# Kernel optimization log

Measured on AMD Instinct MI355X. Metric: run time of the kernel, lower is better.

## Reference

```python
import jax, jax.numpy as jnp
import numpy as np
from jax import lax

LBDA = 0.1
EPS = 0.01
NUM_CLASSES = 20


def setup_inputs() -> dict:
    key = jax.random.key(0)
    k1, k2 = jax.random.split(key)
    target_features = jax.random.normal(k1, (2048, 8, 2048), dtype=jnp.float32)
    support_features = jax.random.normal(k2, (100, 8, 2048), dtype=jnp.float32)
    # 20-way 5-shot: every class present so per-class mean is well defined
    support_labels = jnp.repeat(jnp.arange(NUM_CLASSES, dtype=jnp.int32), 100 // NUM_CLASSES)
    return {
        "target_features": target_features,
        "support_features": support_features,
        "support_labels": support_labels,
    }


def _softmin(xs, lbda):
    # -lbda * log(sum_i exp(-x_i/lbda)), stable
    return -lbda * jax.nn.logsumexp(jnp.stack([-x / lbda for x in xs], axis=0), axis=0)


def otam_cum_dist(dists, lbda=LBDA):
    # dists: [Q, Sp, L, S] frame distance matrices
    d = jnp.pad(dists, ((0, 0), (0, 0), (0, 0), (1, 1)))  # pad columns -> M = S + 2
    M = d.shape[-1]
    # row 0: running sum along columns (cum[0,0] = d[0,0] = 0 from padding)
    row0 = jnp.cumsum(d[:, :, 0, :], axis=-1)

    def step(prev_row, d_row):
        # prev_row, d_row: [Q, Sp, M]; column 0 is never written -> stays 0
        cur = [jnp.zeros_like(d_row[..., 0])]
        cur.append(d_row[..., 1] + _softmin([prev_row[..., 0], prev_row[..., 1], cur[0]], lbda))
        for m in range(2, M - 1):
            cur.append(d_row[..., m] + _softmin([prev_row[..., m - 1], cur[m - 1]], lbda))
        cur.append(d_row[..., M - 1] + _softmin([prev_row[..., M - 2], prev_row[..., M - 1], cur[M - 2]], lbda))
        new_row = jnp.stack(cur, axis=-1)
        return new_row, None

    d_rows = jnp.moveaxis(d[:, :, 1:, :], 2, 0)  # [L-1, Q, Sp, M]
    final_row, _ = lax.scan(step, row0, d_rows)
    return final_row[..., -1]  # [Q, Sp]


def cos_sim(x, y, eps=EPS):
    num = x @ y.T
    den = jnp.linalg.norm(x, axis=-1)[:, None] * jnp.linalg.norm(y, axis=-1)[None, :] + eps
    return num / den


def reference(target_features, support_features, support_labels):
    Q, S, D = target_features.shape
    Sp = support_features.shape[0]
    tf = target_features.reshape(Q * S, D)
    sf = support_features.reshape(Sp * S, D)
    frame_dists = 1.0 - cos_sim(tf, sf)  # [Q*S, Sp*S]
    # '(tb ts) (sb ss) -> tb sb ts ss'
    dists = frame_dists.reshape(Q, S, Sp, S).transpose(0, 2, 1, 3)
    cum_dists = otam_cum_dist(dists) + otam_cum_dist(dists.transpose(0, 1, 3, 2))  # [Q, Sp]
    # per-class mean over support (torch.unique returns sorted labels 0..C-1)
    onehot = (support_labels[:, None] == jnp.arange(NUM_CLASSES)[None, :]).astype(cum_dists.dtype)
    onehot = onehot / jnp.sum(onehot, axis=0, keepdims=True)
    class_dists = cum_dists @ onehot  # [Q, C]
    return -class_dists[None]  # logits [1, Q, C]
```

## Files before the change

kernel.cpp:

```cpp
#include <hip/hip_runtime.h>

#define QN    2048
#define SS    8
#define DD    2048
#define SP    100
#define NCLS  20
#define MROWS (QN*SS)
#define NREAL (SP*SS)
#define NPAD  1024
#define KK    DD
#define BK    64
#define NTK   (KK/BK)

typedef __bf16 bf16x8 __attribute__((ext_vector_type(8)));
typedef float  f32x4  __attribute__((ext_vector_type(4)));

__device__ __forceinline__ unsigned short f2bf(float f) {
    unsigned int u = __float_as_uint(f);
    u += 0x7fffu + ((u >> 16) & 1u);
    return (unsigned short)(u >> 16);
}

__global__ void cvt_kernel(const float* __restrict__ tf, const float* __restrict__ sf,
                           unsigned short* __restrict__ Abf, unsigned short* __restrict__ Bbf,
                           float* __restrict__ nA, float* __restrict__ nB,
                           float* __restrict__ out)
{
    if (blockIdx.x < 160) out[blockIdx.x * 256 + threadIdx.x] = 0.f;

    const int wv   = threadIdx.x >> 6;
    const int lane = threadIdx.x & 63;
    const int row  = blockIdx.x * 4 + wv;

    const float* src;
    unsigned short* dst;
    float* nrm; int r;
    if (row < MROWS) { src = tf + (size_t)row * DD; dst = Abf + (size_t)row * DD; nrm = nA; r = row; }
    else {
        r = row - MROWS;
        if (r >= NREAL) {
            unsigned short* d2 = Bbf + (size_t)r * DD;
            ushort4 z = make_ushort4(0, 0, 0, 0);
#pragma unroll
            for (int j = 0; j < 8; ++j) *(ushort4*)(d2 + j * 256 + lane * 4) = z;
            if (lane == 0) nB[r] = 0.f;
            return;
        }
        src = sf + (size_t)r * DD; dst = Bbf + (size_t)r * DD; nrm = nB;
    }

    float s = 0.f;
#pragma unroll
    for (int j = 0; j < 8; j++) {
        float4 v = *(const float4*)(src + j * 256 + lane * 4);
        s += v.x*v.x + v.y*v.y + v.z*v.z + v.w*v.w;
        ushort4 pk = make_ushort4(f2bf(v.x), f2bf(v.y), f2bf(v.z), f2bf(v.w));
        *(ushort4*)(dst + j * 256 + lane * 4) = pk;
    }
#pragma unroll
    for (int o = 32; o; o >>= 1) s += __shfl_down(s, o);
    if (lane == 0) nrm[r] = sqrtf(s);
}

__device__ __forceinline__ float softmin2(float a, float b) {
    float mn = fminf(a, b), mx = fmaxf(a, b);
    return mn - 0.1f * __logf(1.0f + __expf((mn - mx) * 10.0f));
}
__device__ __forceinline__ float softmin3(float a, float b, float c) {
    float mn = fminf(fminf(a, b), c);
    float sum = __expf((mn - a) * 10.0f) + __expf((mn - b) * 10.0f) + __expf((mn - c) * 10.0f);
    return mn - 0.1f * __logf(sum);
}

__device__ __forceinline__ void gld16(const void* g, void* l) {
    __builtin_amdgcn_global_load_lds(
        (const __attribute__((address_space(1))) unsigned int*)g,
        (__attribute__((address_space(3))) unsigned int*)l, 16, 0, 0);
}

__device__ __forceinline__ float cellf(const uint4* raw, int a, int b) {
    const unsigned* p = (const unsigned*)raw;
    unsigned wv = p[a * 4 + (b >> 1)];
    return __uint_as_float((b & 1) ? (wv & 0xffff0000u) : (wv << 16));
}

__device__ __forceinline__ float otam_dp(const uint4* raw, int dir) {
    float prev[10], cur[10];
    prev[0] = 0.f;
#pragma unroll
    for (int m = 1; m <= 8; m++) {
        float v0 = cellf(raw, 0, m - 1), v1 = cellf(raw, m - 1, 0);
        prev[m] = prev[m - 1] + (dir ? v1 : v0);
    }
    prev[9] = prev[8];
#pragma unroll
    for (int l = 1; l < 8; l++) {
        float d[8];
#pragma unroll
        for (int j = 0; j < 8; j++) {
            float v0 = cellf(raw, l, j), v1 = cellf(raw, j, l);
            d[j] = dir ? v1 : v0;
        }
        cur[1] = d[0] + softmin3(prev[0], prev[1], 0.0f);
#pragma unroll
        for (int m = 2; m <= 8; m++)
            cur[m] = d[m - 1] + softmin2(prev[m - 1], cur[m - 1]);
        cur[9] = softmin3(prev[8], prev[9], cur[8]);
#pragma unroll
        for (int m = 1; m < 10; m++) prev[m] = cur[m];
    }
    return prev[9];
}

template<int CB>
__device__ __forceinline__ void tile_body(
    char* lds8, f32x4 (&acc)[8][4],
    const unsigned short* sA, const unsigned short* sB,
    const int t, const int arow, const int brow, const int sb16, const int stoff)
{
    constexpr int NB = CB ^ 65536;
    const bool st = (t + 1 < NTK);
    const int t1 = (t + 1) * BK;
    bf16x8 bf0[4], bf1[4];

    if (st) {
        gld16(sB + t1,                    lds8 + NB + 32768 + stoff);
        gld16(sB + (size_t) 64 * KK + t1, lds8 + NB + 32768 +  8192 + stoff);
        gld16(sB + (size_t)128 * KK + t1, lds8 + NB + 32768 + 16384 + stoff);
        gld16(sB + (size_t)192 * KK + t1, lds8 + NB + 32768 + 24576 + stoff);
        gld16(sA + t1,                    lds8 + NB + stoff);
        gld16(sA + (size_t)128 * KK + t1, lds8 + NB + 16384 + stoff);
    }

    {
        bf16x8 af0[4], af1[4];
#pragma unroll
        for (int i = 0; i < 4; ++i)
            af0[i] = *(const bf16x8*)(lds8 + CB + arow + i * 2048 + sb16);
#pragma unroll
        for (int n = 0; n < 4; ++n)
            bf0[n] = *(const bf16x8*)(lds8 + CB + brow + n * 2048 + sb16);
#pragma unroll
        for (int i = 0; i < 4; ++i)
            af1[i] = *(const bf16x8*)(lds8 + CB + arow + i * 2048 + (sb16 ^ 64));
#pragma unroll
        for (int n = 0; n < 4; ++n)
            bf1[n] = *(const bf16x8*)(lds8 + CB + brow + n * 2048 + (sb16 ^ 64));
        __builtin_amdgcn_s_setprio(1);
#pragma unroll
        for (int mi = 0; mi < 4; ++mi)
#pragma unroll
            for (int n = 0; n < 4; ++n)
                acc[mi][n] = __builtin_amdgcn_mfma_f32_16x16x32_bf16(af0[mi], bf0[n], acc[mi][n], 0, 0, 0);
#pragma unroll
        for (int mi = 0; mi < 4; ++mi)
#pragma unroll
            for (int n = 0; n < 4; ++n)
                acc[mi][n] = __builtin_amdgcn_mfma_f32_16x16x32_bf16(af1[mi], bf1[n], acc[mi][n], 0, 0, 0);
        __builtin_amdgcn_s_setprio(0);
    }

    if (st) asm volatile("s_waitcnt vmcnt(6)");
    else    asm volatile("s_waitcnt vmcnt(0)");
    __builtin_amdgcn_s_barrier();

    if (st) {
        gld16(sA + (size_t) 64 * KK + t1, lds8 + NB +  8192 + stoff);
        gld16(sA + (size_t)192 * KK + t1, lds8 + NB + 24576 + stoff);
    }

    {
        bf16x8 af2[4], af3[4];
#pragma unroll
        for (int i = 0; i < 4; ++i)
            af2[i] = *(const bf16x8*)(lds8 + CB + arow + 8192 + i * 2048 + sb16);
#pragma unroll
        for (int i = 0; i < 4; ++i)
            af3[i] = *(const bf16x8*)(lds8 + CB + arow + 8192 + i * 2048 + (sb16 ^ 64));
        __builtin_amdgcn_s_setprio(1);
#pragma unroll
        for (int mi = 0; mi < 4; ++mi)
#pragma unroll
            for (int n = 0; n < 4; ++n)
                acc[4 + mi][n] = __builtin_amdgcn_mfma_f32_16x16x32_bf16(af2[mi], bf0[n], acc[4 + mi][n], 0, 0, 0);
#pragma unroll
        for (int mi = 0; mi < 4; ++mi)
#pragma unroll
            for (int n = 0; n < 4; ++n)
                acc[4 + mi][n] = __builtin_amdgcn_mfma_f32_16x16x32_bf16(af3[mi], bf1[n], acc[4 + mi][n], 0, 0, 0);
        __builtin_amdgcn_s_setprio(0);
    }

    if (st) asm volatile("s_waitcnt vmcnt(2)");
    __builtin_amdgcn_s_barrier();
}

__global__ __launch_bounds__(512, 2) void gemm_kernel(
    const unsigned short* __restrict__ A,
    const unsigned short* __restrict__ B,
    const float* __restrict__ nA, const float* __restrict__ nB,
    const int* __restrict__ labels,
    float* __restrict__ out)
{
    extern __shared__ __align__(16) char lds8[];

    const int mt   = blockIdx.x;
    const int nt   = blockIdx.y;
    const int tid  = threadIdx.x;
    const int lane = tid & 63;
    const int w    = tid >> 6;
    const int wm   = w >> 2, wn = w & 3;
    const int col  = lane & 15, kg = lane >> 4;
    const int mbase = mt * 256, nbase = nt * 256;

    const int ks8 = ((lane & 7) ^ (lane >> 3)) << 3;
    const unsigned short* sA = A + (size_t)(mbase + w * 8 + (lane >> 3)) * KK + ks8;
    const unsigned short* sB = B + (size_t)(nbase + w * 8 + (lane >> 3)) * KK + ks8;
    const int stoff = w * 1024 + lane * 16;

    const int sb16 = ((kg ^ (col & 7)) << 4);
    const int arow = (wm * 128 + col) * 128;
    const int brow = 32768 + (wn * 64 + col) * 128;

    f32x4 acc[8][4] = {};

    gld16(sB,                       lds8 + 32768 + stoff);
    gld16(sB + (size_t) 64 * KK,    lds8 + 32768 +  8192 + stoff);
    gld16(sB + (size_t)128 * KK,    lds8 + 32768 + 16384 + stoff);
    gld16(sB + (size_t)192 * KK,    lds8 + 32768 + 24576 + stoff);
    gld16(sA,                       lds8 + stoff);
    gld16(sA + (size_t)128 * KK,    lds8 + 16384 + stoff);
    gld16(sA + (size_t) 64 * KK,    lds8 +  8192 + stoff);
    gld16(sA + (size_t)192 * KK,    lds8 + 24576 + stoff);
    asm volatile("s_waitcnt vmcnt(0)");
    __builtin_amdgcn_s_barrier();

    for (int t = 0; t < NTK; t += 2) {
        tile_body<0>    (lds8, acc, sA, sB, t,     arow, brow, sb16, stoff);
        tile_body<65536>(lds8, acc, sA, sB, t + 1, arow, brow, sb16, stoff);
    }

    __syncthreads();
    unsigned short* eb = (unsigned short*)lds8 + w * 2304;
    const int pr  = lane & 31;
    const int qv2 = pr >> 3, sv = pr & 7;
    const int dir = lane >> 5;

#pragma unroll
    for (int p = 0; p < 4; ++p) {
        if (p) __syncthreads();
#pragma unroll
        for (int mi2 = 0; mi2 < 2; ++mi2) {
            const int mi = p * 2 + mi2;
            float nx[4];
#pragma unroll
            for (int r = 0; r < 4; ++r) nx[r] = nA[mbase + wm * 128 + mi * 16 + kg * 4 + r];
#pragma unroll
            for (int ni = 0; ni < 4; ++ni) {
                const float ny = nB[nbase + wn * 64 + ni * 16 + col];
#pragma unroll
                for (int r = 0; r < 4; ++r) {
                    float d = 1.0f - acc[mi][ni][r] * __builtin_amdgcn_rcpf(nx[r] * ny + 0.01f);
                    eb[(mi2 * 16 + kg * 4 + r) * 72 + ni * 16 + col] = f2bf(d);
                }
            }
        }
        __syncthreads();

        uint4 raw[8];
        const unsigned short* tb = eb + (qv2 * 8) * 72 + sv * 8;
#pragma unroll
        for (int l = 0; l < 8; ++l) raw[l] = *(const uint4*)(tb + l * 72);

        float res = otam_dp(raw, dir);
        res += __shfl_down(res, 32);
        if (dir == 0) {
            const int sg = nt * 32 + wn * 8 + sv;
            if (sg < SP) {
                const int qg = mt * 32 + wm * 16 + p * 4 + qv2;
                atomicAdd(out + (size_t)qg * NCLS + labels[sg], -res * 0.2f);
            }
        }
    }
}

extern "C" void kernel_launch(void* const* d_in, const int* in_sizes, int n_in,
                              void* d_out, int out_size, void* d_ws, size_t ws_size,
                              hipStream_t stream)
{
    const float* tf     = (const float*)d_in[0];
    const float* sf     = (const float*)d_in[1];
    const int*   labels = (const int*)d_in[2];
    float* out = (float*)d_out;

    char* ws = (char*)d_ws;
    const size_t szA    = (size_t)MROWS * KK * 2;
    const size_t szB    = (size_t)NPAD  * KK * 2;
    const size_t szNA   = (size_t)MROWS * 4;
    unsigned short* Abf = (unsigned short*)ws;
    unsigned short* Bbf = (unsigned short*)(ws + szA);
    float* nA   = (float*)(ws + szA + szB);
    float* nB   = (float*)(ws + szA + szB + szNA);

    static int inited = 0;
    if (!inited) {
        (void)hipFuncSetAttribute((const void*)gemm_kernel,
                                  hipFuncAttributeMaxDynamicSharedMemorySize, 131072);
        inited = 1;
    }

    cvt_kernel<<<(MROWS + NPAD) / 4, 256, 0, stream>>>(tf, sf, Abf, Bbf, nA, nB, out);
    gemm_kernel<<<dim3(MROWS / 256, NPAD / 256), 512, 131072, stream>>>(Abf, Bbf, nA, nB, labels, out);
}
```

Before: 282.2 us.

## Shrink GEMM tile to 128x256 with BK=32 triple-buffered LDS pipeline

Restructures the bf16 MFMA GEMM: the block tile drops from 256x256 to 128x256, K-step from 64 to 32, and the double buffer becomes a three-stage LDS ring prefetching two tiles ahead. LDS use falls from 128KB to 72KB and launch bounds allow more resident blocks per CU, aiming for better occupancy and latency hiding. The cost is lower arithmetic intensity per block, more barriers per K, and twice as many blocks reloading B tiles. The epilogue indexing is adjusted to match the smaller M tile.

Result: slower. 289.7 us (+2.7%).

```diff
diff --git a/kernel.cpp b/kernel.cpp
--- a/kernel.cpp
+++ b/kernel.cpp
@@ -9,8 +9,10 @@
 #define NREAL (SP*SS)
 #define NPAD  1024
 #define KK    DD
-#define BK    64
+#define BK    32
 #define NTK   (KK/BK)
+#define BUF   24576
+#define LDSZ  (3*BUF)
 
 typedef __bf16 bf16x8 __attribute__((ext_vector_type(8)));
 typedef float  f32x4  __attribute__((ext_vector_type(4)));
@@ -112,90 +114,39 @@
     return prev[9];
 }
 
-template<int CB>
+template<int CB, int SB>
 __device__ __forceinline__ void tile_body(
-    char* lds8, f32x4 (&acc)[8][4],
-    const unsigned short* sA, const unsigned short* sB,
-    const int t, const int arow, const int brow, const int sb16, const int stoff)
-{
-    constexpr int NB = CB ^ 65536;
-    const bool st = (t + 1 < NTK);
-    const int t1 = (t + 1) * BK;
-    bf16x8 bf0[4], bf1[4];
-
+    char* lds8, f32x4 (&acc)[4][4],
+    const unsigned short* sA, const unsigned short* sB0, const unsigned short* sB1,
+    const int t, const int abase, const int bbase,
+    const int stA, const int stB0, const int stB1)
+{
+    const bool st = (t + 2) < NTK;
+    const int tS = (t + 2) * BK;
     if (st) {
-        gld16(sB + t1,                    lds8 + NB + 32768 + stoff);
-        gld16(sB + (size_t) 64 * KK + t1, lds8 + NB + 32768 +  8192 + stoff);
-        gld16(sB + (size_t)128 * KK + t1, lds8 + NB + 32768 + 16384 + stoff);
-        gld16(sB + (size_t)192 * KK + t1, lds8 + NB + 32768 + 24576 + stoff);
-        gld16(sA + t1,                    lds8 + NB + stoff);
-        gld16(sA + (size_t)128 * KK + t1, lds8 + NB + 16384 + stoff);
-    }
-
-    {
-        bf16x8 af0[4], af1[4];
-#pragma unroll
-        for (int i = 0; i < 4; ++i)
-            af0[i] = *(const bf16x8*)(lds8 + CB + arow + i * 2048 + sb16);
+        gld16(sA  + tS, lds8 + SB + stA);
+        gld16(sB0 + tS, lds8 + SB + stB0);
+        gld16(sB1 + tS, lds8 + SB + stB1);
+    }
+    bf16x8 bf[4];
+#pragma unroll
+    for (int n = 0; n < 4; ++n)
+        bf[n] = *(const bf16x8*)(lds8 + CB + bbase + n * 1024);
+    __builtin_amdgcn_s_setprio(1);
+#pragma unroll
+    for (int mi = 0; mi < 4; ++mi) {
+        bf16x8 af = *(const bf16x8*)(lds8 + CB + abase + mi * 1024);
 #pragma unroll
         for (int n = 0; n < 4; ++n)
-            bf0[n] = *(const bf16x8*)(lds8 + CB + brow + n * 2048 + sb16);
-#pragma unroll
-        for (int i = 0; i < 4; ++i)
-            af1[i] = *(const bf16x8*)(lds8 + CB + arow + i * 2048 + (sb16 ^ 64));
-#pragma unroll
-        for (int n = 0; n < 4; ++n)
-            bf1[n] = *(const bf16x8*)(lds8 + CB + brow + n * 2048 + (sb16 ^ 64));
-        __builtin_amdgcn_s_setprio(1);
-#pragma unroll
-        for (int mi = 0; mi < 4; ++mi)
-#pragma unroll
-            for (int n = 0; n < 4; ++n)
-                acc[mi][n] = __builtin_amdgcn_mfma_f32_16x16x32_bf16(af0[mi], bf0[n], acc[mi][n], 0, 0, 0);
-#pragma unroll
-        for (int mi = 0; mi < 4; ++mi)
-#pragma unroll
-            for (int n = 0; n < 4; ++n)
-                acc[mi][n] = __builtin_amdgcn_mfma_f32_16x16x32_bf16(af1[mi], bf1[n], acc[mi][n], 0, 0, 0);
-        __builtin_amdgcn_s_setprio(0);
-    }
-
-    if (st) asm volatile("s_waitcnt vmcnt(6)");
-    else    asm volatile("s_waitcnt vmcnt(0)");
+            acc[mi][n] = __builtin_amdgcn_mfma_f32_16x16x32_bf16(af, bf[n], acc[mi][n], 0, 0, 0);
+    }
+    __builtin_amdgcn_s_setprio(0);
+    if (st)                 asm volatile("s_waitcnt vmcnt(3)");
+    else if (t + 1 < NTK)   asm volatile("s_waitcnt vmcnt(0)");
     __builtin_amdgcn_s_barrier();
-
-    if (st) {
-        gld16(sA + (size_t) 64 * KK + t1, lds8 + NB +  8192 + stoff);
-        gld16(sA + (size_t)192 * KK + t1, lds8 + NB + 24576 + stoff);
-    }
-
-    {
-        bf16x8 af2[4], af3[4];
-#pragma unroll
-        for (int i = 0; i < 4; ++i)
-            af2[i] = *(const bf16x8*)(lds8 + CB + arow + 8192 + i * 2048 + sb16);
-#pragma unroll
-        for (int i = 0; i < 4; ++i)
-            af3[i] = *(const bf16x8*)(lds8 + CB + arow + 8192 + i * 2048 + (sb16 ^ 64));
-        __builtin_amdgcn_s_setprio(1);
-#pragma unroll
-        for (int mi = 0; mi < 4; ++mi)
-#pragma unroll
-            for (int n = 0; n < 4; ++n)
-                acc[4 + mi][n] = __builtin_amdgcn_mfma_f32_16x16x32_bf16(af2[mi], bf0[n], acc[4 + mi][n], 0, 0, 0);
-#pragma unroll
-        for (int mi = 0; mi < 4; ++mi)
-#pragma unroll
-            for (int n = 0; n < 4; ++n)
-                acc[4 + mi][n] = __builtin_amdgcn_mfma_f32_16x16x32_bf16(af3[mi], bf1[n], acc[4 + mi][n], 0, 0, 0);
-        __builtin_amdgcn_s_setprio(0);
-    }
-
-    if (st) asm volatile("s_waitcnt vmcnt(2)");
-    __builtin_amdgcn_s_barrier();
-}
-
-__global__ __launch_bounds__(512, 2) void gemm_kernel(
+}
+
+__global__ __launch_bounds__(512, 4) void gemm_kernel(
     const unsigned short* __restrict__ A,
     const unsigned short* __restrict__ B,
     const float* __restrict__ nA, const float* __restrict__ nB,
@@ -211,50 +162,50 @@
     const int w    = tid >> 6;
     const int wm   = w >> 2, wn = w & 3;
     const int col  = lane & 15, kg = lane >> 4;
-    const int mbase = mt * 256, nbase = nt * 256;
-
-    const int ks8 = ((lane & 7) ^ (lane >> 3)) << 3;
-    const unsigned short* sA = A + (size_t)(mbase + w * 8 + (lane >> 3)) * KK + ks8;
-    const unsigned short* sB = B + (size_t)(nbase + w * 8 + (lane >> 3)) * KK + ks8;
-    const int stoff = w * 1024 + lane * 16;
-
-    const int sb16 = ((kg ^ (col & 7)) << 4);
-    const int arow = (wm * 128 + col) * 128;
-    const int brow = 32768 + (wn * 64 + col) * 128;
-
-    f32x4 acc[8][4] = {};
-
-    gld16(sB,                       lds8 + 32768 + stoff);
-    gld16(sB + (size_t) 64 * KK,    lds8 + 32768 +  8192 + stoff);
-    gld16(sB + (size_t)128 * KK,    lds8 + 32768 + 16384 + stoff);
-    gld16(sB + (size_t)192 * KK,    lds8 + 32768 + 24576 + stoff);
-    gld16(sA,                       lds8 + stoff);
-    gld16(sA + (size_t)128 * KK,    lds8 + 16384 + stoff);
-    gld16(sA + (size_t) 64 * KK,    lds8 +  8192 + stoff);
-    gld16(sA + (size_t)192 * KK,    lds8 + 24576 + stoff);
-    asm volatile("s_waitcnt vmcnt(0)");
+    const int mbase = mt * 128, nbase = nt * 256;
+
+    const int srow = tid >> 2;
+    const int sks  = ((tid & 3) ^ ((tid >> 3) & 3)) << 3;
+    const unsigned short* sA  = A + (size_t)(mbase + srow) * KK + sks;
+    const unsigned short* sB0 = B + (size_t)(nbase + srow) * KK + sks;
+    const unsigned short* sB1 = B + (size_t)(nbase + 128 + srow) * KK + sks;
+    const int stA  = tid * 16;
+    const int stB0 = 8192  + tid * 16;
+    const int stB1 = 16384 + tid * 16;
+
+    const int arow0 = wm * 64 + col;
+    const int abase = arow0 * 64 + ((kg ^ ((col >> 1) & 3)) << 4);
+    const int brow0 = wn * 64 + col;
+    const int bbase = 8192 + brow0 * 64 + ((kg ^ ((col >> 1) & 3)) << 4);
+
+    f32x4 acc[4][4] = {};
+
+    gld16(sA,       lds8 + stA);  gld16(sB0,       lds8 + stB0);  gld16(sB1,       lds8 + stB1);
+    gld16(sA + BK,  lds8 + BUF + stA); gld16(sB0 + BK, lds8 + BUF + stB0); gld16(sB1 + BK, lds8 + BUF + stB1);
+    asm volatile("s_waitcnt vmcnt(3)");
     __builtin_amdgcn_s_barrier();
 
-    for (int t = 0; t < NTK; t += 2) {
-        tile_body<0>    (lds8, acc, sA, sB, t,     arow, brow, sb16, stoff);
-        tile_body<65536>(lds8, acc, sA, sB, t + 1, arow, brow, sb16, stoff);
-    }
-
-    __syncthreads();
+    for (int t = 0; t < NTK - 1; t += 3) {
+        tile_body<0,     2*BUF>(lds8, acc, sA, sB0, sB1, t,     abase, bbase, stA, stB0, stB1);
+        tile_body<BUF,   0    >(lds8, acc, sA, sB0, sB1, t + 1, abase, bbase, stA, stB0, stB1);
+        tile_body<2*BUF, BUF  >(lds8, acc, sA, sB0, sB1, t + 2, abase, bbase, stA, stB0, stB1);
+    }
+    tile_body<0, 2*BUF>(lds8, acc, sA, sB0, sB1, NTK - 1, abase, bbase, stA, stB0, stB1);
+
     unsigned short* eb = (unsigned short*)lds8 + w * 2304;
     const int pr  = lane & 31;
     const int qv2 = pr >> 3, sv = pr & 7;
     const int dir = lane >> 5;
 
 #pragma unroll
-    for (int p = 0; p < 4; ++p) {
+    for (int p = 0; p < 2; ++p) {
         if (p) __syncthreads();
 #pragma unroll
         for (int mi2 = 0; mi2 < 2; ++mi2) {
             const int mi = p * 2 + mi2;
             float nx[4];
 #pragma unroll
-            for (int r = 0; r < 4; ++r) nx[r] = nA[mbase + wm * 128 + mi * 16 + kg * 4 + r];
+            for (int r = 0; r < 4; ++r) nx[r] = nA[mbase + wm * 64 + mi * 16 + kg * 4 + r];
 #pragma unroll
             for (int ni = 0; ni < 4; ++ni) {
                 const float ny = nB[nbase + wn * 64 + ni * 16 + col];
@@ -277,7 +228,7 @@
         if (dir == 0) {
             const int sg = nt * 32 + wn * 8 + sv;
             if (sg < SP) {
-                const int qg = mt * 32 + wm * 16 + p * 4 + qv2;
+                const int qg = mt * 16 + wm * 8 + p * 4 + qv2;
                 atomicAdd(out + (size_t)qg * NCLS + labels[sg], -res * 0.2f);
             }
         }
@@ -305,10 +256,10 @@
     static int inited = 0;
     if (!inited) {
         (void)hipFuncSetAttribute((const void*)gemm_kernel,
-                                  hipFuncAttributeMaxDynamicSharedMemorySize, 131072);
+                                  hipFuncAttributeMaxDynamicSharedMemorySize, LDSZ);
         inited = 1;
     }
 
     cvt_kernel<<<(MROWS + NPAD) / 4, 256, 0, stream>>>(tf, sf, Abf, Bbf, nA, nB, out);
-    gemm_kernel<<<dim3(MROWS / 256, NPAD / 256), 512, 131072, stream>>>(Abf, Bbf, nA, nB, labels, out);
-}
+    gemm_kernel<<<dim3(MROWS / 128, NPAD / 256), 512, LDSZ, stream>>>(Abf, Bbf, nA, nB, labels, out);
+}
```
